# Optimization experiments

Measured on AMD Instinct MI355X. Metric: run time of the kernel, lower is better.

## Reference

```python
import jax, jax.numpy as jnp
import numpy as np

G, N, E, D, B, L, CL = 4, 100000, 1600000, 64, 32, 50, 2


def setup_inputs() -> dict:
    key = jax.random.key(0)
    ks = jax.random.split(key, 20)
    w = lambda k, s: jax.random.normal(k, s, dtype=jnp.float32) * 0.05
    return {
        'src': jax.random.randint(ks[0], (G, E), 0, N, dtype=jnp.int32),
        'dst': jax.random.randint(ks[1], (G, E), 0, N, dtype=jnp.int32),
        'ew': jax.random.uniform(ks[2], (G, E), dtype=jnp.float32),
        'emb': jax.random.normal(ks[3], (G, N, D), dtype=jnp.float32),
        'Wself1': w(ks[4], (G, D, D)), 'Wneigh1': w(ks[5], (G, D, D)),
        'b1': jnp.zeros((G, D), jnp.float32),
        'Wself2': w(ks[6], (G, D, D)), 'Wneigh2': w(ks[7], (G, D, D)),
        'b2': jnp.zeros((G, D), jnp.float32),
        'Q1': w(ks[8], (CL, D, D)), 'K1': w(ks[9], (CL, D, D)), 'V1': w(ks[10], (CL, D, D)),
        'Q2': w(ks[11], (CL, D, D)), 'K2': w(ks[12], (CL, D, D)), 'V2': w(ks[13], (CL, D, D)),
        'cand_idx': jax.random.randint(ks[14], (B, G, L), 0, N, dtype=jnp.int32),
    }


def _sage_conv(feat, src, dst, ew, Ws, Wn, b):
    # DGL SAGEConv 'mean' with edge_weight: neigh = mean over incoming edges of (h_src * w_e)
    n = feat.shape[0]
    msg = feat[src] * ew[:, None]                       # [E, D]
    summed = jax.ops.segment_sum(msg, dst, num_segments=n)
    deg = jax.ops.segment_sum(jnp.ones_like(ew), dst, num_segments=n)
    neigh = summed / jnp.maximum(deg, 1.0)[:, None]
    return feat @ Ws.T + neigh @ Wn.T + b


def _attn(x, Wq, Wk, Wv):
    q = x @ Wq.T
    k = x @ Wk.T
    v = x @ Wv.T
    scale = 1.0 / jnp.sqrt(jnp.float32(x.shape[-1]))
    s = jnp.einsum('...ld,...md->...lm', q, k) * scale
    return jax.nn.softmax(s, axis=-1) @ v


def reference(src, dst, ew, emb, Wself1, Wneigh1, b1, Wself2, Wneigh2, b2,
              Q1, K1, V1, Q2, K2, V2, cand_idx):
    def gnn(feat, s, d, w_e, ws1, wn1, bb1, ws2, wn2, bb2):
        h = jax.nn.relu(_sage_conv(feat, s, d, w_e, ws1, wn1, bb1))
        return _sage_conv(h, s, d, w_e, ws2, wn2, bb2)

    node_emb = jax.vmap(gnn)(emb, src, dst, ew,
                             Wself1, Wneigh1, b1, Wself2, Wneigh2, b2)  # [G, N, D]

    g = emb.shape[0]
    sel = node_emb[jnp.arange(g)[None, :, None], cand_idx]  # [B, G, L, D]

    x = sel
    for i in range(Q1.shape[0]):
        x = _attn(x, Q1[i], K1[i], V1[i])
    x = x.sum(axis=-2)  # [B, G, D]
    for i in range(Q2.shape[0]):
        x = _attn(x, Q2[i], K2[i], V2[i])
    return x.sum(axis=-2)  # [B, D]
```

## Files before the change

kernel.cpp:

```cpp
#include <hip/hip_runtime.h>
#include <cstdint>
#include <cstddef>
#include <cmath>

#define NN   100000
#define NE   1600000
#define DD   64
#define NG   4
#define NB_  32
#define NL   50
#define NCL  2
#define SCAN_NB 49
#define STRIDE 80
#define ROWCAP 32768
#define WPAD 68

__global__ __launch_bounds__(256) void k_wt(const float* __restrict__ Ws,
                                            const float* __restrict__ Wn,
                                            float* __restrict__ wt, int g0) {
    const int gy = blockIdx.y;
    const int g = g0 + gy;
    float* o = wt + (size_t)gy * 2 * DD * DD;
    int i = blockIdx.x * 256 + threadIdx.x;
    if (i < DD * DD) {
        int r = i >> 6, k = i & 63;
        o[k * DD + r] = Ws[(size_t)g * DD * DD + r * DD + k];
        o[DD * DD + k * DD + r] = Wn[(size_t)g * DD * DD + r * DD + k];
    }
}

__global__ __launch_bounds__(256) void k_candmark(const int* __restrict__ cand,
                                                  int* __restrict__ candbm,
                                                  int* __restrict__ mark, int g0) {
    const int gy = blockIdx.y;
    const int g = g0 + gy;
    int t = blockIdx.x * 256 + threadIdx.x;
    if (t < NB_ * NL) {
        int b = t / NL, l = t - b * NL;
        int n = cand[((size_t)b * NG + g) * NL + l];
        candbm[(size_t)gy * NN + n] = 1;
        mark[(size_t)gy * NN + n] = 1;
    }
}

__global__ __launch_bounds__(256) void k_mark2(const int* __restrict__ src,
                                               const int* __restrict__ dst,
                                               const int* __restrict__ candbm,
                                               int* __restrict__ mark, int g0) {
    const int gy = blockIdx.y;
    const int g = g0 + gy;
    int q = blockIdx.x * 256 + threadIdx.x;
    if (q < NE / 4) {
        int4 dv = ((const int4*)(dst + (size_t)g * NE))[q];
        int4 sv = ((const int4*)(src + (size_t)g * NE))[q];
        const int* cb = candbm + (size_t)gy * NN;
        int* mk = mark + (size_t)gy * NN;
        if (cb[dv.x]) mk[sv.x] = 1;
        if (cb[dv.y]) mk[sv.y] = 1;
        if (cb[dv.z]) mk[sv.z] = 1;
        if (cb[dv.w]) mk[sv.w] = 1;
    }
}

__global__ __launch_bounds__(256) void k_cscan1(const int* __restrict__ mark,
                                                int* __restrict__ partc) {
    const int gy = blockIdx.y;
    const int* m = mark + (size_t)gy * NN;
    __shared__ int sh[256];
    const int tid = threadIdx.x;
    int base = blockIdx.x * 2048 + tid * 8;
    int s = 0;
    for (int i = 0; i < 8; ++i) { int idx = base + i; if (idx < NN) s += m[idx]; }
    sh[tid] = s; __syncthreads();
    for (int off = 128; off > 0; off >>= 1) {
        if (tid < off) sh[tid] += sh[tid + off];
        __syncthreads();
    }
    if (tid == 0) partc[gy * 64 + blockIdx.x] = sh[0];
}

__global__ __launch_bounds__(256) void k_cscan3(const int* __restrict__ mark,
                                                const int* __restrict__ partc,
                                                int* __restrict__ list,
                                                int* __restrict__ rank,
                                                int* __restrict__ nlist) {
    const int gy = blockIdx.y;
    const int* m = mark + (size_t)gy * NN;
    int* li = list + (size_t)gy * NN;
    int* rk = rank + (size_t)gy * NN;
    __shared__ int sh[256];
    __shared__ int sbase;
    const int tid = threadIdx.x;
    if (tid == 0) {
        int b = 0;
        for (int i = 0; i < blockIdx.x; ++i) b += partc[gy * 64 + i];
        sbase = b;
    }
    int base = blockIdx.x * 2048 + tid * 8;
    int vals[8];
    int s = 0;
    for (int i = 0; i < 8; ++i) {
        int idx = base + i;
        int v = (idx < NN) ? m[idx] : 0;
        vals[i] = v; s += v;
    }
    sh[tid] = s; __syncthreads();
    for (int off = 1; off < 256; off <<= 1) {
        int t = (tid >= off) ? sh[tid - off] : 0;
        __syncthreads();
        sh[tid] += t;
        __syncthreads();
    }
    int excl = sh[tid] - s;
    int run = sbase + excl;
    for (int i = 0; i < 8; ++i) {
        int idx = base + i;
        if (idx < NN) {
            if (vals[i]) { li[run] = idx; rk[idx] = run + 1; ++run; }
            else rk[idx] = 0;
        }
    }
    if (blockIdx.x == SCAN_NB - 1 && tid == 255) nlist[gy] = sbase + sh[255];
}

__global__ __launch_bounds__(256) void k_scatter3(const int* __restrict__ src,
                                                  const int* __restrict__ dst,
                                                  const float* __restrict__ ew,
                                                  const int* __restrict__ rank,
                                                  int* __restrict__ cur,
                                                  int2* __restrict__ edf, int g0) {
    const int gy = blockIdx.y;
    const int g = g0 + gy;
    int q = blockIdx.x * 256 + threadIdx.x;
    if (q < NE / 4) {
        int4   dv = ((const int4*)(dst + (size_t)g * NE))[q];
        int4   sv = ((const int4*)(src + (size_t)g * NE))[q];
        float4 wv = ((const float4*)(ew + (size_t)g * NE))[q];
        const int* rk = rank + (size_t)gy * NN;
        int* cu = cur + (size_t)gy * ROWCAP;
        int2* ef = edf + (size_t)gy * ROWCAP * STRIDE;
        int r0 = rk[dv.x] - 1;
        if (r0 >= 0 && r0 < ROWCAP) { int p = atomicAdd(&cu[r0], 1); if (p < STRIDE) ef[(size_t)r0 * STRIDE + p] = make_int2(sv.x, __float_as_int(wv.x)); }
        int r1 = rk[dv.y] - 1;
        if (r1 >= 0 && r1 < ROWCAP) { int p = atomicAdd(&cu[r1], 1); if (p < STRIDE) ef[(size_t)r1 * STRIDE + p] = make_int2(sv.y, __float_as_int(wv.y)); }
        int r2 = rk[dv.z] - 1;
        if (r2 >= 0 && r2 < ROWCAP) { int p = atomicAdd(&cu[r2], 1); if (p < STRIDE) ef[(size_t)r2 * STRIDE + p] = make_int2(sv.z, __float_as_int(wv.z)); }
        int r3 = rk[dv.w] - 1;
        if (r3 >= 0 && r3 < ROWCAP) { int p = atomicAdd(&cu[r3], 1); if (p < STRIDE) ef[(size_t)r3 * STRIDE + p] = make_int2(sv.w, __float_as_int(wv.w)); }
    }
}

__global__ __launch_bounds__(256) void k_conv_full(
    const float* __restrict__ emb, const int2* __restrict__ edf,
    const int* __restrict__ cur, const float* __restrict__ wt,
    const float* __restrict__ bias, float* __restrict__ outh,
    const int* __restrict__ list, const int* __restrict__ nlist,
    const int* __restrict__ rawsrc, const int* __restrict__ rawdst,
    const float* __restrict__ rawew, int g0)
{
    const int gy = blockIdx.y;
    const int g = g0 + gy;
    const float* feat = emb + (size_t)g * NN * DD;
    const int2* ed = edf + (size_t)gy * ROWCAP * STRIDE;
    const int* cu = cur + (size_t)gy * ROWCAP;
    const int* li = list + (size_t)gy * NN;
    const float* wsT = wt + (size_t)gy * 2 * DD * DD;
    const float* wnT = wsT + DD * DD;
    float* og = outh + (size_t)gy * ROWCAP * DD;
    const int lane = threadIdx.x & 63;
    const int wid = threadIdx.x >> 6;

    __shared__ __attribute__((aligned(16))) float fs[4][16][DD];
    __shared__ __attribute__((aligned(16))) float ns[4][16][DD];

    const float bv = bias[(size_t)g * DD + lane];
    const int nl = min(nlist[gy], ROWCAP);
    const int wglob = blockIdx.x * 4 + wid;
    const int wstep = gridDim.x * 4;
    for (int tb = wglob * 16; tb < nl; tb += wstep * 16) {
        const int nrows = min(16, nl - tb);
        int nL = 0, cL = 0;
        if (lane < nrows) { nL = li[tb + lane]; cL = cu[tb + lane]; }
        for (int r = 0; r < nrows; ++r) {
            const int n = __shfl(nL, r);
            const int cnt = __shfl(cL, r);
            fs[wid][r][lane] = feat[(size_t)n * DD + lane];
            float acc = 0.f;
            if (cnt <= STRIDE) {
                const int c64 = min(cnt, 64);
                int myS = 0; float myW = 0.f;
                if (lane < c64) {
                    int2 e = ed[(size_t)(tb + r) * STRIDE + lane];
                    myS = e.x; myW = __int_as_float(e.y);
                }
                for (int j = 0; j < c64; j += 8) {
                    float fv[8], wv[8];
#pragma unroll
                    for (int u = 0; u < 8; ++u) {
                        int s = __shfl(myS, j + u);
                        wv[u] = __shfl(myW, j + u);
                        fv[u] = feat[(size_t)s * DD + lane];
                    }
#pragma unroll
                    for (int u = 0; u < 8; ++u) acc = fmaf(fv[u], wv[u], acc);
                }
                for (int j = 64; j < cnt; ++j) {
                    int2 e = ed[(size_t)(tb + r) * STRIDE + j];
                    acc = fmaf(feat[(size_t)e.x * DD + lane], __int_as_float(e.y), acc);
                }
            } else {
                for (int base = 0; base < NE; base += 64) {
                    int d = rawdst[(size_t)g * NE + base + lane];
                    int s = rawsrc[(size_t)g * NE + base + lane];
                    float w = rawew[(size_t)g * NE + base + lane];
                    unsigned long long mball = __ballot(d == n);
                    while (mball) {
                        int i = __ffsll(mball) - 1; mball &= mball - 1;
                        acc = fmaf(feat[(size_t)__shfl(s, i) * DD + lane], __shfl(w, i), acc);
                    }
                }
            }
            ns[wid][r][lane] = acc / fmaxf((float)cnt, 1.f);
        }
        float o[16];
#pragma unroll
        for (int r = 0; r < 16; ++r) o[r] = bv;
        for (int k4 = 0; k4 < 16; ++k4) {
            float ws0 = wsT[(4 * k4 + 0) * DD + lane];
            float ws1 = wsT[(4 * k4 + 1) * DD + lane];
            float ws2 = wsT[(4 * k4 + 2) * DD + lane];
            float ws3 = wsT[(4 * k4 + 3) * DD + lane];
            float wn0 = wnT[(4 * k4 + 0) * DD + lane];
            float wn1 = wnT[(4 * k4 + 1) * DD + lane];
            float wn2 = wnT[(4 * k4 + 2) * DD + lane];
            float wn3 = wnT[(4 * k4 + 3) * DD + lane];
#pragma unroll
            for (int r = 0; r < 16; ++r) {
                float4 f  = *(const float4*)&fs[wid][r][4 * k4];
                float4 nv = *(const float4*)&ns[wid][r][4 * k4];
                o[r] = fmaf(ws0, f.x,  o[r]);
                o[r] = fmaf(ws1, f.y,  o[r]);
                o[r] = fmaf(ws2, f.z,  o[r]);
                o[r] = fmaf(ws3, f.w,  o[r]);
                o[r] = fmaf(wn0, nv.x, o[r]);
                o[r] = fmaf(wn1, nv.y, o[r]);
                o[r] = fmaf(wn2, nv.z, o[r]);
                o[r] = fmaf(wn3, nv.w, o[r]);
            }
        }
#pragma unroll
        for (int r = 0; r < 16; ++r)
            if (r < nrows) og[(size_t)(tb + r) * DD + lane] = fmaxf(o[r], 0.f);
    }
}

__global__ __launch_bounds__(256) void k_conv_cand(
    const float* __restrict__ hfeat, const int2* __restrict__ edf,
    const int* __restrict__ cur, const int* __restrict__ rank,
    const float* __restrict__ Wsf, const float* __restrict__ Wng,
    const float* __restrict__ bias, const int* __restrict__ cand,
    const int* __restrict__ rawsrc, const int* __restrict__ rawdst,
    const float* __restrict__ rawew,
    float* __restrict__ sel, int g0)
{
    const int gy = blockIdx.y;
    const int g = g0 + gy;
    const float* feat = hfeat + (size_t)gy * ROWCAP * DD;
    const int2* ed = edf + (size_t)gy * ROWCAP * STRIDE;
    const int* cu = cur + (size_t)gy * ROWCAP;
    const int* rk = rank + (size_t)gy * NN;
    const int lane = threadIdx.x & 63;
    const int wid = threadIdx.x >> 6;

    __shared__ __attribute__((aligned(16))) float lws[DD][WPAD];
    __shared__ __attribute__((aligned(16))) float lwn[DD][WPAD];
    __shared__ __attribute__((aligned(16))) float fs[4][DD];
    __shared__ __attribute__((aligned(16))) float nsh[4][DD];

    for (int i = threadIdx.x; i < DD * 16; i += 256) {
        int row = i >> 4, blk = i & 15;
        *(float4*)&lws[row][blk * 4] = *(const float4*)(Wsf + (size_t)g * DD * DD + (size_t)row * DD + blk * 4);
        *(float4*)&lwn[row][blk * 4] = *(const float4*)(Wng + (size_t)g * DD * DD + (size_t)row * DD + blk * 4);
    }
    __syncthreads();
    const float bv = bias[(size_t)g * DD + lane];

    int t = blockIdx.x * 4 + wid;
    if (t < NB_ * NL) {
        int b = t / NL;
        int l = t - b * NL;
        int n = cand[((size_t)b * NG + g) * NL + l];
        const int rc = rk[n] - 1;
        const int cnt = cu[rc];
        const float fself = feat[(size_t)rc * DD + lane];
        float acc = 0.f;
        if (cnt <= STRIDE) {
            const int c64 = min(cnt, 64);
            int myS = 0; float myW = 0.f;
            if (lane < c64) {
                int2 e = ed[(size_t)rc * STRIDE + lane];
                myS = rk[e.x] - 1;
                myW = __int_as_float(e.y);
            }
            for (int j = 0; j < c64; j += 8) {
                float fv[8], wv[8];
#pragma unroll
                for (int u = 0; u < 8; ++u) {
                    int s = __shfl(myS, j + u);
                    wv[u] = __shfl(myW, j + u);
                    fv[u] = feat[(size_t)max(s, 0) * DD + lane];
                }
#pragma unroll
                for (int u = 0; u < 8; ++u) acc = fmaf(fv[u], wv[u], acc);
            }
            for (int j = 64; j < cnt; ++j) {
                int2 e = ed[(size_t)rc * STRIDE + j];
                int s = rk[e.x] - 1;
                acc = fmaf(feat[(size_t)max(s, 0) * DD + lane], __int_as_float(e.y), acc);
            }
        } else {
            for (int base = 0; base < NE; base += 64) {
                int d = rawdst[(size_t)g * NE + base + lane];
                int s = rawsrc[(size_t)g * NE + base + lane];
                float w = rawew[(size_t)g * NE + base + lane];
                unsigned long long mball = __ballot(d == n);
                while (mball) {
                    int i = __ffsll(mball) - 1; mball &= mball - 1;
                    int si = __shfl(s, i);
                    int srank = rk[si] - 1;
                    acc = fmaf(feat[(size_t)max(srank, 0) * DD + lane], __shfl(w, i), acc);
                }
            }
        }
        float neigh = acc / fmaxf((float)cnt, 1.f);
        fs[wid][lane] = fself;
        nsh[wid][lane] = neigh;
        float o = bv;
#pragma unroll
        for (int k4 = 0; k4 < 16; ++k4) {
            float4 ws4 = *(const float4*)&lws[lane][k4 * 4];
            float4 wn4 = *(const float4*)&lwn[lane][k4 * 4];
            float4 f  = *(const float4*)&fs[wid][k4 * 4];
            float4 nv = *(const float4*)&nsh[wid][k4 * 4];
            o = fmaf(ws4.x, f.x,  o);
            o = fmaf(ws4.y, f.y,  o);
            o = fmaf(ws4.z, f.z,  o);
            o = fmaf(ws4.w, f.w,  o);
            o = fmaf(wn4.x, nv.x, o);
            o = fmaf(wn4.y, nv.y, o);
            o = fmaf(wn4.z, nv.z, o);
            o = fmaf(wn4.w, nv.w, o);
        }
        sel[(((size_t)b * NG + g) * NL + l) * DD + lane] = o;
    }
}

__global__ __launch_bounds__(256) void k_attn1(
    const float* __restrict__ sel, const float* __restrict__ Q,
    const float* __restrict__ K, const float* __restrict__ V,
    float* __restrict__ xsum)
{
    __shared__ __attribute__((aligned(16))) float x[NL * DD];
    __shared__ __attribute__((aligned(16))) float qp[NL * 68];
    __shared__ __attribute__((aligned(16))) float kk[NL * 68];
    const int tid = threadIdx.x;
    const int lane = tid & 63;
    const int wid = tid >> 6;
    const int bg = blockIdx.x;
    const float* xin = sel + (size_t)bg * NL * DD;
    for (int i = tid; i < NL * DD; i += 256) x[i] = xin[i];
    __syncthreads();

    for (int layer = 0; layer < NCL; ++layer) {
        const float* Qb = Q + (size_t)layer * DD * DD;
        const float* Kb = K + (size_t)layer * DD * DD;
        const float* Vb = V + (size_t)layer * DD * DD;
        float wrow[DD];
#pragma unroll
        for (int k4 = 0; k4 < 16; ++k4) {
            float4 a = *(const float4*)(Qb + (size_t)lane * DD + 4 * k4);
            wrow[4 * k4 + 0] = a.x; wrow[4 * k4 + 1] = a.y; wrow[4 * k4 + 2] = a.z; wrow[4 * k4 + 3] = a.w;
        }
        for (int l = wid; l < NL; l += 4) {
            float acc = 0.f;
#pragma unroll
            for (int k4 = 0; k4 < 16; ++k4) {
                float4 xv = *(const float4*)&x[l * DD + 4 * k4];
                acc = fmaf(wrow[4 * k4 + 0], xv.x, acc);
                acc = fmaf(wrow[4 * k4 + 1], xv.y, acc);
                acc = fmaf(wrow[4 * k4 + 2], xv.z, acc);
                acc = fmaf(wrow[4 * k4 + 3], xv.w, acc);
            }
            qp[l * 68 + lane] = acc;
        }
#pragma unroll
        for (int k4 = 0; k4 < 16; ++k4) {
            float4 a = *(const float4*)(Kb + (size_t)lane * DD + 4 * k4);
            wrow[4 * k4 + 0] = a.x; wrow[4 * k4 + 1] = a.y; wrow[4 * k4 + 2] = a.z; wrow[4 * k4 + 3] = a.w;
        }
        for (int l = wid; l < NL; l += 4) {
            float acc = 0.f;
#pragma unroll
            for (int k4 = 0; k4 < 16; ++k4) {
                float4 xv = *(const float4*)&x[l * DD + 4 * k4];
                acc = fmaf(wrow[4 * k4 + 0], xv.x, acc);
                acc = fmaf(wrow[4 * k4 + 1], xv.y, acc);
                acc = fmaf(wrow[4 * k4 + 2], xv.z, acc);
                acc = fmaf(wrow[4 * k4 + 3], xv.w, acc);
            }
            kk[l * 68 + lane] = acc;
        }
        __syncthreads();
        for (int l = wid; l < NL; l += 4) {
            float s;
            if (lane < NL) {
                float acc = 0.f;
#pragma unroll
                for (int k4 = 0; k4 < 16; ++k4) {
                    float4 qv = *(const float4*)&qp[l * 68 + 4 * k4];
                    float4 kv = *(const float4*)&kk[lane * 68 + 4 * k4];
                    acc += qv.x * kv.x + qv.y * kv.y + qv.z * kv.z + qv.w * kv.w;
                }
                s = acc * 0.125f;
            } else {
                s = -INFINITY;
            }
            float mx = s;
#pragma unroll
            for (int m = 32; m >= 1; m >>= 1) mx = fmaxf(mx, __shfl_xor(mx, m));
            float pe = __expf(s - mx);
            float sm = pe;
#pragma unroll
            for (int m = 32; m >= 1; m >>= 1) sm += __shfl_xor(sm, m);
            qp[l * 68 + lane] = pe / sm;
        }
        __syncthreads();
        for (int l = wid; l < NL; l += 4) {
            float acc = 0.f;
            for (int m = 0; m < NL; ++m)
                acc = fmaf(qp[l * 68 + m], x[m * DD + lane], acc);
            kk[l * 68 + lane] = acc;
        }
        __syncthreads();
#pragma unroll
        for (int k4 = 0; k4 < 16; ++k4) {
            float4 a = *(const float4*)(Vb + (size_t)lane * DD + 4 * k4);
            wrow[4 * k4 + 0] = a.x; wrow[4 * k4 + 1] = a.y; wrow[4 * k4 + 2] = a.z; wrow[4 * k4 + 3] = a.w;
        }
        for (int l = wid; l < NL; l += 4) {
            float acc = 0.f;
#pragma unroll
            for (int k4 = 0; k4 < 16; ++k4) {
                float4 yv = *(const float4*)&kk[l * 68 + 4 * k4];
                acc = fmaf(wrow[4 * k4 + 0], yv.x, acc);
                acc = fmaf(wrow[4 * k4 + 1], yv.y, acc);
                acc = fmaf(wrow[4 * k4 + 2], yv.z, acc);
                acc = fmaf(wrow[4 * k4 + 3], yv.w, acc);
            }
            x[l * DD + lane] = acc;
        }
        __syncthreads();
    }
    if (wid == 0) {
        float acc = 0.f;
        for (int l = 0; l < NL; ++l) acc += x[l * DD + lane];
        xsum[(size_t)bg * DD + lane] = acc;
    }
}

__global__ __launch_bounds__(64) void k_attn2(
    const float* __restrict__ xin, const float* __restrict__ Q,
    const float* __restrict__ K, const float* __restrict__ V,
    float* __restrict__ out)
{
    __shared__ __attribute__((aligned(16))) float x[NG * DD];
    const int j = threadIdx.x;
    const int b = blockIdx.x;
    for (int i = j; i < NG * DD; i += 64) x[i] = xin[(size_t)b * NG * DD + i];
    __syncthreads();
    float o[NG];
    for (int layer = 0; layer < NCL; ++layer) {
        float wrow[DD];
        float q4[NG], k4v[NG], v4[NG];
        const float* Qb = Q + (size_t)layer * DD * DD + (size_t)j * DD;
        const float* Kb = K + (size_t)layer * DD * DD + (size_t)j * DD;
        const float* Vb = V + (size_t)layer * DD * DD + (size_t)j * DD;
#pragma unroll
        for (int k4 = 0; k4 < 16; ++k4) {
            float4 a = *(const float4*)(Qb + 4 * k4);
            wrow[4 * k4 + 0] = a.x; wrow[4 * k4 + 1] = a.y; wrow[4 * k4 + 2] = a.z; wrow[4 * k4 + 3] = a.w;
        }
#pragma unroll
        for (int g = 0; g < NG; ++g) {
            float acc = 0.f;
#pragma unroll
            for (int k4 = 0; k4 < 16; ++k4) {
                float4 xv = *(const float4*)&x[g * DD + 4 * k4];
                acc = fmaf(wrow[4 * k4 + 0], xv.x, acc);
                acc = fmaf(wrow[4 * k4 + 1], xv.y, acc);
                acc = fmaf(wrow[4 * k4 + 2], xv.z, acc);
                acc = fmaf(wrow[4 * k4 + 3], xv.w, acc);
            }
            q4[g] = acc;
        }
#pragma unroll
        for (int k4 = 0; k4 < 16; ++k4) {
            float4 a = *(const float4*)(Kb + 4 * k4);
            wrow[4 * k4 + 0] = a.x; wrow[4 * k4 + 1] = a.y; wrow[4 * k4 + 2] = a.z; wrow[4 * k4 + 3] = a.w;
        }
#pragma unroll
        for (int g = 0; g < NG; ++g) {
            float acc = 0.f;
#pragma unroll
            for (int k4 = 0; k4 < 16; ++k4) {
                float4 xv = *(const float4*)&x[g * DD + 4 * k4];
                acc = fmaf(wrow[4 * k4 + 0], xv.x, acc);
                acc = fmaf(wrow[4 * k4 + 1], xv.y, acc);
                acc = fmaf(wrow[4 * k4 + 2], xv.z, acc);
                acc = fmaf(wrow[4 * k4 + 3], xv.w, acc);
            }
            k4v[g] = acc;
        }
#pragma unroll
        for (int k4 = 0; k4 < 16; ++k4) {
            float4 a = *(const float4*)(Vb + 4 * k4);
            wrow[4 * k4 + 0] = a.x; wrow[4 * k4 + 1] = a.y; wrow[4 * k4 + 2] = a.z; wrow[4 * k4 + 3] = a.w;
        }
#pragma unroll
        for (int g = 0; g < NG; ++g) {
            float acc = 0.f;
#pragma unroll
            for (int k4 = 0; k4 < 16; ++k4) {
                float4 xv = *(const float4*)&x[g * DD + 4 * k4];
                acc = fmaf(wrow[4 * k4 + 0], xv.x, acc);
                acc = fmaf(wrow[4 * k4 + 1], xv.y, acc);
                acc = fmaf(wrow[4 * k4 + 2], xv.z, acc);
                acc = fmaf(wrow[4 * k4 + 3], xv.w, acc);
            }
            v4[g] = acc;
        }
        float p[NG][NG];
#pragma unroll
        for (int l = 0; l < NG; ++l) {
#pragma unroll
            for (int m = 0; m < NG; ++m) {
                float t = q4[l] * k4v[m];
#pragma unroll
                for (int mk = 32; mk >= 1; mk >>= 1) t += __shfl_xor(t, mk);
                p[l][m] = t * 0.125f;
            }
        }
#pragma unroll
        for (int l = 0; l < NG; ++l) {
            float mx = fmaxf(fmaxf(p[l][0], p[l][1]), fmaxf(p[l][2], p[l][3]));
            float e0 = __expf(p[l][0] - mx), e1 = __expf(p[l][1] - mx);
            float e2 = __expf(p[l][2] - mx), e3 = __expf(p[l][3] - mx);
            float inv = 1.f / (e0 + e1 + e2 + e3);
            o[l] = (e0 * v4[0] + e1 * v4[1] + e2 * v4[2] + e3 * v4[3]) * inv;
        }
        __syncthreads();
#pragma unroll
        for (int l = 0; l < NG; ++l) x[l * DD + j] = o[l];
        __syncthreads();
    }
    out[(size_t)b * DD + j] = o[0] + o[1] + o[2] + o[3];
}

extern "C" void kernel_launch(void* const* d_in, const int* in_sizes, int n_in,
                              void* d_out, int out_size, void* d_ws, size_t ws_size,
                              hipStream_t stream)
{
    const int*   src  = (const int*)  d_in[0];
    const int*   dst  = (const int*)  d_in[1];
    const float* ew   = (const float*)d_in[2];
    const float* emb  = (const float*)d_in[3];
    const float* Ws1  = (const float*)d_in[4];
    const float* Wn1  = (const float*)d_in[5];
    const float* b1   = (const float*)d_in[6];
    const float* Ws2  = (const float*)d_in[7];
    const float* Wn2  = (const float*)d_in[8];
    const float* b2   = (const float*)d_in[9];
    const float* Q1   = (const float*)d_in[10];
    const float* K1   = (const float*)d_in[11];
    const float* V1   = (const float*)d_in[12];
    const float* Q2   = (const float*)d_in[13];
    const float* K2   = (const float*)d_in[14];
    const float* V2   = (const float*)d_in[15];
    const int*   cand = (const int*)  d_in[16];
    float* out = (float*)d_out;

    auto padded = [](size_t b) { return (b + 255) & ~(size_t)255; };
    auto need = [&](int GG) -> size_t {
        size_t s = 0;
        s += padded((size_t)GG * ROWCAP * STRIDE * 8);
        s += padded((size_t)GG * ROWCAP * DD * 4);
        s += padded((size_t)GG * ROWCAP * 4);
        s += padded((size_t)NB_ * NG * NL * DD * 4);
        s += padded((size_t)NB_ * NG * DD * 4);
        s += padded((size_t)GG * NN * 4) * 4;
        s += padded((size_t)GG * 64 * 4) * 2;
        s += padded((size_t)GG * 2 * DD * DD * 4);
        return s;
    };
    const int GG = (ws_size >= need(4)) ? 4 : 1;

    char* p = (char*)d_ws;
    auto alloc = [&](size_t b) -> void* { void* r = (void*)p; p += padded(b); return r; };
    int2*  edf  = (int2*) alloc((size_t)GG * ROWCAP * STRIDE * 8);
    float* hb   = (float*)alloc((size_t)GG * ROWCAP * DD * 4);
    int*   cur  = (int*)  alloc((size_t)GG * ROWCAP * 4);
    float* sel  = (float*)alloc((size_t)NB_ * NG * NL * DD * 4);
    float* xsum = (float*)alloc((size_t)NB_ * NG * DD * 4);
    int*   cbm  = (int*)  alloc((size_t)GG * NN * 4);
    int*   mark = (int*)  alloc((size_t)GG * NN * 4);
    int*   list = (int*)  alloc((size_t)GG * NN * 4);
    int*   rank = (int*)  alloc((size_t)GG * NN * 4);
    int*   prtc = (int*)  alloc((size_t)GG * 64 * 4);
    int*   nlst = (int*)  alloc((size_t)GG * 64 * 4);
    float* wt   = (float*)alloc((size_t)GG * 2 * DD * DD * 4);

    const int QB = (NE / 4 + 255) / 256;
    const int CB = (NB_ * NL + 255) / 256;
    for (int g0 = 0; g0 < NG; g0 += GG) {
        hipMemsetAsync(cbm, 0, (size_t)GG * NN * 4, stream);
        hipMemsetAsync(mark, 0, (size_t)GG * NN * 4, stream);
        hipMemsetAsync(cur, 0, (size_t)GG * ROWCAP * 4, stream);
        k_wt      <<<dim3(16, GG), 256, 0, stream>>>(Ws1, Wn1, wt, g0);
        k_candmark<<<dim3(CB, GG), 256, 0, stream>>>(cand, cbm, mark, g0);
        k_mark2   <<<dim3(QB, GG), 256, 0, stream>>>(src, dst, cbm, mark, g0);
        k_cscan1  <<<dim3(SCAN_NB, GG), 256, 0, stream>>>(mark, prtc);
        k_cscan3  <<<dim3(SCAN_NB, GG), 256, 0, stream>>>(mark, prtc, list, rank, nlst);
        k_scatter3<<<dim3(QB, GG), 256, 0, stream>>>(src, dst, ew, rank, cur, edf, g0);
        k_conv_full<<<dim3(448, GG), 256, 0, stream>>>(emb, edf, cur, wt, b1, hb, list, nlst,
                                                       src, dst, ew, g0);
        k_conv_cand<<<dim3((NB_ * NL) / 4, GG), 256, 0, stream>>>(hb, edf, cur, rank, Ws2, Wn2, b2,
                                                                  cand, src, dst, ew, sel, g0);
    }
    k_attn1<<<NB_ * NG, 256, 0, stream>>>(sel, Q1, K1, V1, xsum);
    k_attn2<<<NB_, 64, 0, stream>>>(xsum, Q2, K2, V2, out);
}
```

Baseline: 356.1 us.

## Shrink conv_full row tiles to four and interleave paired-row neighbor gathers

The first-layer conv kernel now gives each wavefront 4 destination rows instead of 16 and launches 1600 blocks per graph instead of 448, so the work spreads across more wavefronts. Edge records for all four rows are loaded up front, and the neighbor gathers for two rows at a time are interleaved so more independent global loads are in flight at once. The raw-edge scan fallback moves into a helper function. In exchange, each wavefront reuses the weight matrix over fewer rows, so weight loads per output row go up, and register pressure from the paired gathers may rise.

```diff
diff --git a/kernel.cpp b/kernel.cpp
--- a/kernel.cpp
+++ b/kernel.cpp
@@ -150,6 +150,25 @@
     }
 }
 
+__device__ __forceinline__ float conv_raw_fallback(const int* __restrict__ rawsrc,
+                                                   const int* __restrict__ rawdst,
+                                                   const float* __restrict__ rawew,
+                                                   const float* __restrict__ feat,
+                                                   int g, int n, int lane) {
+    float acc = 0.f;
+    for (int base = 0; base < NE; base += 64) {
+        int d = rawdst[(size_t)g * NE + base + lane];
+        int s = rawsrc[(size_t)g * NE + base + lane];
+        float w = rawew[(size_t)g * NE + base + lane];
+        unsigned long long mball = __ballot(d == n);
+        while (mball) {
+            int i = __ffsll(mball) - 1; mball &= mball - 1;
+            acc = fmaf(feat[(size_t)__shfl(s, i) * DD + lane], __shfl(w, i), acc);
+        }
+    }
+    return acc;
+}
+
 __global__ __launch_bounds__(256) void k_conv_full(
     const float* __restrict__ emb, const int2* __restrict__ edf,
     const int* __restrict__ cur, const float* __restrict__ wt,
@@ -170,61 +189,135 @@
     const int lane = threadIdx.x & 63;
     const int wid = threadIdx.x >> 6;
 
-    __shared__ __attribute__((aligned(16))) float fs[4][16][DD];
-    __shared__ __attribute__((aligned(16))) float ns[4][16][DD];
+    __shared__ __attribute__((aligned(16))) float fs[4][4][DD];
+    __shared__ __attribute__((aligned(16))) float ns[4][4][DD];
 
     const float bv = bias[(size_t)g * DD + lane];
     const int nl = min(nlist[gy], ROWCAP);
     const int wglob = blockIdx.x * 4 + wid;
     const int wstep = gridDim.x * 4;
-    for (int tb = wglob * 16; tb < nl; tb += wstep * 16) {
-        const int nrows = min(16, nl - tb);
+    for (int tb = wglob * 4; tb < nl; tb += wstep * 4) {
+        const int nrows = min(4, nl - tb);
         int nL = 0, cL = 0;
         if (lane < nrows) { nL = li[tb + lane]; cL = cu[tb + lane]; }
-        for (int r = 0; r < nrows; ++r) {
-            const int n = __shfl(nL, r);
-            const int cnt = __shfl(cL, r);
-            fs[wid][r][lane] = feat[(size_t)n * DD + lane];
-            float acc = 0.f;
-            if (cnt <= STRIDE) {
-                const int c64 = min(cnt, 64);
-                int myS = 0; float myW = 0.f;
-                if (lane < c64) {
-                    int2 e = ed[(size_t)(tb + r) * STRIDE + lane];
-                    myS = e.x; myW = __int_as_float(e.y);
-                }
-                for (int j = 0; j < c64; j += 8) {
-                    float fv[8], wv[8];
-#pragma unroll
-                    for (int u = 0; u < 8; ++u) {
-                        int s = __shfl(myS, j + u);
-                        wv[u] = __shfl(myW, j + u);
-                        fv[u] = feat[(size_t)s * DD + lane];
+        int2 rec0 = make_int2(0, 0), rec1 = make_int2(0, 0);
+        int2 rec2 = make_int2(0, 0), rec3 = make_int2(0, 0);
+        {
+            int c0 = min(__shfl(cL, 0), 64);
+            if (lane < c0) rec0 = ed[(size_t)(tb + 0) * STRIDE + lane];
+            if (nrows > 1) { int c = min(__shfl(cL, 1), 64); if (lane < c) rec1 = ed[(size_t)(tb + 1) * STRIDE + lane]; }
+            if (nrows > 2) { int c = min(__shfl(cL, 2), 64); if (lane < c) rec2 = ed[(size_t)(tb + 2) * STRIDE + lane]; }
+            if (nrows > 3) { int c = min(__shfl(cL, 3), 64); if (lane < c) rec3 = ed[(size_t)(tb + 3) * STRIDE + lane]; }
+        }
+        fs[wid][0][lane] = feat[(size_t)__shfl(nL, 0) * DD + lane];
+        if (nrows > 1) fs[wid][1][lane] = feat[(size_t)__shfl(nL, 1) * DD + lane];
+        if (nrows > 2) fs[wid][2][lane] = feat[(size_t)__shfl(nL, 2) * DD + lane];
+        if (nrows > 3) fs[wid][3][lane] = feat[(size_t)__shfl(nL, 3) * DD + lane];
+
+        float acc0 = 0.f, acc1 = 0.f, acc2 = 0.f, acc3 = 0.f;
+        {
+            const int cA = min(__shfl(cL, 0), 64);
+            const int cB = (nrows > 1) ? min(__shfl(cL, 1), 64) : 0;
+            const int sA = rec0.x; const float wA = __int_as_float(rec0.y);
+            const int sB = rec1.x; const float wB = __int_as_float(rec1.y);
+            const int lim = max(cA, cB);
+            for (int j = 0; j < lim; j += 8) {
+                float fvA[8], fvB[8];
+                const bool doA = j < cA, doB = j < cB;
+                if (doA) {
+#pragma unroll
+                    for (int u = 0; u < 8; ++u) fvA[u] = feat[(size_t)__shfl(sA, j + u) * DD + lane];
+                }
+                if (doB) {
+#pragma unroll
+                    for (int u = 0; u < 8; ++u) fvB[u] = feat[(size_t)__shfl(sB, j + u) * DD + lane];
+                }
+                if (doA) {
+#pragma unroll
+                    for (int u = 0; u < 8; ++u) acc0 = fmaf(fvA[u], __shfl(wA, j + u), acc0);
+                }
+                if (doB) {
+#pragma unroll
+                    for (int u = 0; u < 8; ++u) acc1 = fmaf(fvB[u], __shfl(wB, j + u), acc1);
+                }
+            }
+        }
+        if (nrows > 2) {
+            const int cA = min(__shfl(cL, 2), 64);
+            const int cB = (nrows > 3) ? min(__shfl(cL, 3), 64) : 0;
+            const int sA = rec2.x; const float wA = __int_as_float(rec2.y);
+            const int sB = rec3.x; const float wB = __int_as_float(rec3.y);
+            const int lim = max(cA, cB);
+            for (int j = 0; j < lim; j += 8) {
+                float fvA[8], fvB[8];
+                const bool doA = j < cA, doB = j < cB;
+                if (doA) {
+#pragma unroll
+                    for (int u = 0; u < 8; ++u) fvA[u] = feat[(size_t)__shfl(sA, j + u) * DD + lane];
+                }
+                if (doB) {
+#pragma unroll
+                    for (int u = 0; u < 8; ++u) fvB[u] = feat[(size_t)__shfl(sB, j + u) * DD + lane];
+                }
+                if (doA) {
+#pragma unroll
+                    for (int u = 0; u < 8; ++u) acc2 = fmaf(fvA[u], __shfl(wA, j + u), acc2);
+                }
+                if (doB) {
+#pragma unroll
+                    for (int u = 0; u < 8; ++u) acc3 = fmaf(fvB[u], __shfl(wB, j + u), acc3);
+                }
+            }
+        }
+        {
+            const int cnt = __shfl(cL, 0);
+            if (cnt > 64) {
+                if (cnt <= STRIDE) {
+                    for (int j = 64; j < cnt; ++j) {
+                        int2 e = ed[(size_t)(tb + 0) * STRIDE + j];
+                        acc0 = fmaf(feat[(size_t)e.x * DD + lane], __int_as_float(e.y), acc0);
                     }
-#pragma unroll
-                    for (int u = 0; u < 8; ++u) acc = fmaf(fv[u], wv[u], acc);
-                }
-                for (int j = 64; j < cnt; ++j) {
-                    int2 e = ed[(size_t)(tb + r) * STRIDE + j];
-                    acc = fmaf(feat[(size_t)e.x * DD + lane], __int_as_float(e.y), acc);
-                }
-            } else {
-                for (int base = 0; base < NE; base += 64) {
-                    int d = rawdst[(size_t)g * NE + base + lane];
-                    int s = rawsrc[(size_t)g * NE + base + lane];
-                    float w = rawew[(size_t)g * NE + base + lane];
-                    unsigned long long mball = __ballot(d == n);
-                    while (mball) {
-                        int i = __ffsll(mball) - 1; mball &= mball - 1;
-                        acc = fmaf(feat[(size_t)__shfl(s, i) * DD + lane], __shfl(w, i), acc);
+                } else acc0 = conv_raw_fallback(rawsrc, rawdst, rawew, feat, g, __shfl(nL, 0), lane);
+            }
+            ns[wid][0][lane] = acc0 / fmaxf((float)cnt, 1.f);
+        }
+        if (nrows > 1) {
+            const int cnt = __shfl(cL, 1);
+            if (cnt > 64) {
+                if (cnt <= STRIDE) {
+                    for (int j = 64; j < cnt; ++j) {
+                        int2 e = ed[(size_t)(tb + 1) * STRIDE + j];
+                        acc1 = fmaf(feat[(size_t)e.x * DD + lane], __int_as_float(e.y), acc1);
                     }
-                }
-            }
-            ns[wid][r][lane] = acc / fmaxf((float)cnt, 1.f);
-        }
-        float o[16];
-#pragma unroll
-        for (int r = 0; r < 16; ++r) o[r] = bv;
+                } else acc1 = conv_raw_fallback(rawsrc, rawdst, rawew, feat, g, __shfl(nL, 1), lane);
+            }
+            ns[wid][1][lane] = acc1 / fmaxf((float)cnt, 1.f);
+        }
+        if (nrows > 2) {
+            const int cnt = __shfl(cL, 2);
+            if (cnt > 64) {
+                if (cnt <= STRIDE) {
+                    for (int j = 64; j < cnt; ++j) {
+                        int2 e = ed[(size_t)(tb + 2) * STRIDE + j];
+                        acc2 = fmaf(feat[(size_t)e.x * DD + lane], __int_as_float(e.y), acc2);
+                    }
+                } else acc2 = conv_raw_fallback(rawsrc, rawdst, rawew, feat, g, __shfl(nL, 2), lane);
+            }
+            ns[wid][2][lane] = acc2 / fmaxf((float)cnt, 1.f);
+        }
+        if (nrows > 3) {
+            const int cnt = __shfl(cL, 3);
+            if (cnt > 64) {
+                if (cnt <= STRIDE) {
+                    for (int j = 64; j < cnt; ++j) {
+                        int2 e = ed[(size_t)(tb + 3) * STRIDE + j];
+                        acc3 = fmaf(feat[(size_t)e.x * DD + lane], __int_as_float(e.y), acc3);
+                    }
+                } else acc3 = conv_raw_fallback(rawsrc, rawdst, rawew, feat, g, __shfl(nL, 3), lane);
+            }
+            ns[wid][3][lane] = acc3 / fmaxf((float)cnt, 1.f);
+        }
+        float o0 = bv, o1 = bv, o2 = bv, o3 = bv;
         for (int k4 = 0; k4 < 16; ++k4) {
             float ws0 = wsT[(4 * k4 + 0) * DD + lane];
             float ws1 = wsT[(4 * k4 + 1) * DD + lane];
@@ -234,23 +327,24 @@
             float wn1 = wnT[(4 * k4 + 1) * DD + lane];
             float wn2 = wnT[(4 * k4 + 2) * DD + lane];
             float wn3 = wnT[(4 * k4 + 3) * DD + lane];
-#pragma unroll
-            for (int r = 0; r < 16; ++r) {
-                float4 f  = *(const float4*)&fs[wid][r][4 * k4];
-                float4 nv = *(const float4*)&ns[wid][r][4 * k4];
-                o[r] = fmaf(ws0, f.x,  o[r]);
-                o[r] = fmaf(ws1, f.y,  o[r]);
-                o[r] = fmaf(ws2, f.z,  o[r]);
-                o[r] = fmaf(ws3, f.w,  o[r]);
-                o[r] = fmaf(wn0, nv.x, o[r]);
-                o[r] = fmaf(wn1, nv.y, o[r]);
-                o[r] = fmaf(wn2, nv.z, o[r]);
-                o[r] = fmaf(wn3, nv.w, o[r]);
-            }
-        }
-#pragma unroll
-        for (int r = 0; r < 16; ++r)
-            if (r < nrows) og[(size_t)(tb + r) * DD + lane] = fmaxf(o[r], 0.f);
+            float4 f, nv;
+            f = *(const float4*)&fs[wid][0][4 * k4]; nv = *(const float4*)&ns[wid][0][4 * k4];
+            o0 = fmaf(ws0, f.x, o0); o0 = fmaf(ws1, f.y, o0); o0 = fmaf(ws2, f.z, o0); o0 = fmaf(ws3, f.w, o0);
+            o0 = fmaf(wn0, nv.x, o0); o0 = fmaf(wn1, nv.y, o0); o0 = fmaf(wn2, nv.z, o0); o0 = fmaf(wn3, nv.w, o0);
+            f = *(const float4*)&fs[wid][1][4 * k4]; nv = *(const float4*)&ns[wid][1][4 * k4];
+            o1 = fmaf(ws0, f.x, o1); o1 = fmaf(ws1, f.y, o1); o1 = fmaf(ws2, f.z, o1); o1 = fmaf(ws3, f.w, o1);
+            o1 = fmaf(wn0, nv.x, o1); o1 = fmaf(wn1, nv.y, o1); o1 = fmaf(wn2, nv.z, o1); o1 = fmaf(wn3, nv.w, o1);
+            f = *(const float4*)&fs[wid][2][4 * k4]; nv = *(const float4*)&ns[wid][2][4 * k4];
+            o2 = fmaf(ws0, f.x, o2); o2 = fmaf(ws1, f.y, o2); o2 = fmaf(ws2, f.z, o2); o2 = fmaf(ws3, f.w, o2);
+            o2 = fmaf(wn0, nv.x, o2); o2 = fmaf(wn1, nv.y, o2); o2 = fmaf(wn2, nv.z, o2); o2 = fmaf(wn3, nv.w, o2);
+            f = *(const float4*)&fs[wid][3][4 * k4]; nv = *(const float4*)&ns[wid][3][4 * k4];
+            o3 = fmaf(ws0, f.x, o3); o3 = fmaf(ws1, f.y, o3); o3 = fmaf(ws2, f.z, o3); o3 = fmaf(ws3, f.w, o3);
+            o3 = fmaf(wn0, nv.x, o3); o3 = fmaf(wn1, nv.y, o3); o3 = fmaf(wn2, nv.z, o3); o3 = fmaf(wn3, nv.w, o3);
+        }
+        og[(size_t)(tb + 0) * DD + lane] = fmaxf(o0, 0.f);
+        if (nrows > 1) og[(size_t)(tb + 1) * DD + lane] = fmaxf(o1, 0.f);
+        if (nrows > 2) og[(size_t)(tb + 2) * DD + lane] = fmaxf(o2, 0.f);
+        if (nrows > 3) og[(size_t)(tb + 3) * DD + lane] = fmaxf(o3, 0.f);
     }
 }
 
@@ -631,8 +725,8 @@
         k_cscan1  <<<dim3(SCAN_NB, GG), 256, 0, stream>>>(mark, prtc);
         k_cscan3  <<<dim3(SCAN_NB, GG), 256, 0, stream>>>(mark, prtc, list, rank, nlst);
         k_scatter3<<<dim3(QB, GG), 256, 0, stream>>>(src, dst, ew, rank, cur, edf, g0);
-        k_conv_full<<<dim3(448, GG), 256, 0, stream>>>(emb, edf, cur, wt, b1, hb, list, nlst,
-                                                       src, dst, ew, g0);
+        k_conv_full<<<dim3(1600, GG), 256, 0, stream>>>(emb, edf, cur, wt, b1, hb, list, nlst,
+                                                        src, dst, ew, g0);
         k_conv_cand<<<dim3((NB_ * NL) / 4, GG), 256, 0, stream>>>(hb, edf, cur, rank, Ws2, Wn2, b2,
                                                                   cand, src, dst, ew, sel, g0);
     }
```

Measured after the change: 355.2 us. No clear change (-0.2%).
